# Kernel optimization log

Hardware: AMD Instinct MI355X
Metric: run time of the kernel (lower is better)

The kernel has to match this reference:

```python
import jax, jax.numpy as jnp
import numpy as np

B, S, D, H, FF = 2, 2048, 1024, 16, 4096
HD = D // H          # head dim = 64
ROT = HD // 2        # rotary dim = dim/(num_heads*2) = 32 (partial rotation)
EPS = 1e-5


def setup_inputs() -> dict:
    key = jax.random.key(0)
    ks = jax.random.split(key, 16)
    std = 0.02
    return {
        "x": jax.random.normal(ks[0], (B, S, D), jnp.float32),
        "mask": jnp.ones((B, 1, 1, S), jnp.int32),
        "wq": jax.random.normal(ks[1], (D, D), jnp.float32) * std,
        "bq": jnp.zeros((D,), jnp.float32),
        "wk": jax.random.normal(ks[2], (D, D), jnp.float32) * std,
        "bk": jnp.zeros((D,), jnp.float32),
        "wv": jax.random.normal(ks[3], (D, D), jnp.float32) * std,
        "bv": jnp.zeros((D,), jnp.float32),
        "wo": jax.random.normal(ks[4], (D, D), jnp.float32) * std,
        "bo": jnp.zeros((D,), jnp.float32),
        "ln1_w": jnp.ones((D,), jnp.float32),
        "ln1_b": jnp.zeros((D,), jnp.float32),
        "ln2_w": jnp.ones((D,), jnp.float32),
        "ln2_b": jnp.zeros((D,), jnp.float32),
        "w1": jax.random.normal(ks[5], (D, FF), jnp.float32) * std,
        "b1": jnp.zeros((FF,), jnp.float32),
        "w2": jax.random.normal(ks[6], (FF, D), jnp.float32) * std,
        "b2": jnp.zeros((D,), jnp.float32),
    }


def _layernorm(x, w, b):
    mu = jnp.mean(x, axis=-1, keepdims=True)
    var = jnp.mean(jnp.square(x - mu), axis=-1, keepdims=True)
    return (x - mu) * jax.lax.rsqrt(var + EPS) * w + b


def _rope(t):
    # t: [B, H, S, HD]; rotate first ROT features, interleaved (GPT-J) pairing
    inv_freq = 1.0 / (10000.0 ** (jnp.arange(0, ROT, 2, dtype=jnp.float32) / ROT))
    ang = jnp.arange(S, dtype=jnp.float32)[:, None] * inv_freq      # [S, ROT//2]
    ang = jnp.repeat(ang, 2, axis=-1)                               # [S, ROT]
    cos, sin = jnp.cos(ang), jnp.sin(ang)
    t_rot, t_pass = t[..., :ROT], t[..., ROT:]
    pr = t_rot.reshape(*t_rot.shape[:-1], ROT // 2, 2)
    rot = jnp.stack([-pr[..., 1], pr[..., 0]], axis=-1).reshape(t_rot.shape)
    return jnp.concatenate([t_rot * cos + rot * sin, t_pass], axis=-1)


def reference(x, mask, wq, bq, wk, bk, wv, bv, wo, bo,
              ln1_w, ln1_b, ln2_w, ln2_b, w1, b1, w2, b2):
    res = x
    h = _layernorm(x, ln1_w, ln1_b)
    q = (h @ wq + bq).reshape(B, S, H, HD).transpose(0, 2, 1, 3)
    k = (h @ wk + bk).reshape(B, S, H, HD).transpose(0, 2, 1, 3)
    v = (h @ wv + bv).reshape(B, S, H, HD).transpose(0, 2, 1, 3)
    q, k = _rope(q), _rope(k)
    score = jnp.einsum('bhqd,bhkd->bhqk', q, k) * (1.0 / np.sqrt(HD))
    score = jnp.where(mask == 0, jnp.float32(-1e9), score)
    attn = jax.nn.softmax(score, axis=-1)
    out = jnp.einsum('bhqk,bhkd->bhqd', attn, v)
    out = out.transpose(0, 2, 1, 3).reshape(B, S, D) @ wo + bo
    x = res + out
    res = x
    h = _layernorm(x, ln2_w, ln2_b)
    h = jax.nn.gelu(h @ w1 + b1, approximate=False) @ w2 + b2
    return res + h
```

## Files before the change

### kernel.cpp

```cpp
#include <hip/hip_runtime.h>
#include <cstdint>
#include <cstddef>


typedef __bf16 bf16;
typedef __bf16 bf16x2 __attribute__((ext_vector_type(2)));
typedef __bf16 bf16x4v __attribute__((ext_vector_type(4)));
typedef __bf16 bf16x8 __attribute__((ext_vector_type(8)));
typedef float  f32x4  __attribute__((ext_vector_type(4)));

#define NB 2
#define NS 2048
#define ND 1024
#define NH 16
#define NHD 64
#define NFF 4096
#define NM (NB*NS)
#define QKSCALE 0.18033688011112042f

typedef uint32_t __attribute__((address_space(1))) gu32_t;
typedef uint32_t __attribute__((address_space(3))) lu32_t;
__device__ __forceinline__ void async_copy16(void* lds, const void* g) {
  __builtin_amdgcn_global_load_lds((gu32_t*)g, (lu32_t*)lds, 16, 0, 0);
}

__device__ __forceinline__ float gelu_f(float x) {
  return 0.5f * x * (1.0f + erff(x * 0.70710678118654752f));
}

__global__ __launch_bounds__(256) void prep_kernel(
    const float* __restrict__ wq, const float* __restrict__ wk,
    const float* __restrict__ wv, const float* __restrict__ wo,
    const float* __restrict__ w1, const float* __restrict__ w2,
    bf16* __restrict__ wqt, bf16* __restrict__ wkt, bf16* __restrict__ wvt,
    bf16* __restrict__ wot, bf16* __restrict__ w1t, bf16* __restrict__ w2t,
    const float* __restrict__ bq, const float* __restrict__ bk,
    const float* __restrict__ bv, float* __restrict__ bcat,
    const int* __restrict__ mask, float* __restrict__ m01f,
    bf16* __restrict__ m01b, float2* __restrict__ rtab,
    const float* __restrict__ x, const float* __restrict__ ln1w,
    const float* __restrict__ ln1b, bf16* __restrict__ h1) {
  int flat = blockIdx.x;
  int t = threadIdx.x;
  if (flat < 12288) {
    __shared__ float tile[32][33];
    const float* W; bf16* Wt; long bx, by; int K, N;
    if (flat < 4096) {
      int which = flat >> 10, r = flat & 1023;
      const float* Ws[4] = {wq, wk, wv, wo};
      bf16* Wts[4] = {wqt, wkt, wvt, wot};
      W = Ws[which]; Wt = Wts[which]; bx = r & 31; by = r >> 5; K = ND; N = ND;
    } else if (flat < 8192) {
      int r = flat - 4096;
      W = w1; Wt = w1t; bx = r & 127; by = r >> 7; K = ND; N = NFF;
    } else {
      int r = flat - 8192;
      W = w2; Wt = w2t; bx = r & 31; by = r >> 5; K = NFF; N = ND;
    }
    int tx = t & 31, ty = t >> 5;
#pragma unroll
    for (int r = 0; r < 4; ++r)
      tile[ty + r*8][tx] = W[(by*32 + ty + r*8) * (long)N + bx*32 + tx];
    __syncthreads();
#pragma unroll
    for (int r = 0; r < 4; ++r)
      Wt[(bx*32 + ty + r*8) * (long)K + by*32 + tx] = (bf16)tile[tx][ty + r*8];
  } else if (flat < 12444) {
    int blk = flat - 12288;
    if (blk < 12) {
      int i = blk * 256 + t;
      bcat[i] = (i < ND) ? bq[i] : ((i < 2*ND) ? bk[i - ND] : bv[i - 2*ND]);
    } else if (blk < 28) {
      int i = (blk - 12) * 256 + t;
      float v = mask[i] ? 1.0f : 0.0f;
      m01f[i] = v;
      m01b[i] = (bf16)v;
    } else {
      int idx = (blk - 28) * 256 + t;
      int s = idx >> 4, i = idx & 15;
      float ang = (float)s * exp2f(-(float)i * (13.287712379549449f / 16.0f));
      float sn, cs;
      sincosf(ang, &sn, &cs);
      rtab[idx] = make_float2(cs, sn);
    }
  } else {
    long row = flat - 12444;
    float4 v = ((const float4*)(x + row*ND))[t];
    float s  = v.x + v.y + v.z + v.w;
    float sq = v.x*v.x + v.y*v.y + v.z*v.z + v.w*v.w;
#pragma unroll
    for (int m = 1; m <= 32; m <<= 1) { s += __shfl_xor(s, m); sq += __shfl_xor(sq, m); }
    __shared__ float ss[4], ssq[4];
    if ((t & 63) == 0) { ss[t>>6] = s; ssq[t>>6] = sq; }
    __syncthreads();
    s  = ss[0] + ss[1] + ss[2] + ss[3];
    sq = ssq[0] + ssq[1] + ssq[2] + ssq[3];
    float mu = s * (1.0f/ND);
    float rs = rsqrtf(sq * (1.0f/ND) - mu*mu + 1e-5f);
    float4 wv4 = ((const float4*)ln1w)[t];
    float4 bv4 = ((const float4*)ln1b)[t];
    bf16x4v o;
    o[0] = (bf16)((v.x-mu)*rs*wv4.x + bv4.x);
    o[1] = (bf16)((v.y-mu)*rs*wv4.y + bv4.y);
    o[2] = (bf16)((v.z-mu)*rs*wv4.z + bv4.z);
    o[3] = (bf16)((v.w-mu)*rs*wv4.w + bv4.w);
    *(bf16x4v*)(h1 + row*ND + t*4) = o;
  }
}

__global__ __launch_bounds__(256) void ln_kernel(
    const float* __restrict__ x, const float* __restrict__ w,
    const float* __restrict__ b, bf16* __restrict__ out) {
  long row = blockIdx.x;
  int t = threadIdx.x;
  float4 v = ((const float4*)(x + row*ND))[t];
  float s  = v.x + v.y + v.z + v.w;
  float sq = v.x*v.x + v.y*v.y + v.z*v.z + v.w*v.w;
#pragma unroll
  for (int m = 1; m <= 32; m <<= 1) { s += __shfl_xor(s, m); sq += __shfl_xor(sq, m); }
  __shared__ float ss[4], ssq[4];
  if ((t & 63) == 0) { ss[t>>6] = s; ssq[t>>6] = sq; }
  __syncthreads();
  s  = ss[0] + ss[1] + ss[2] + ss[3];
  sq = ssq[0] + ssq[1] + ssq[2] + ssq[3];
  float mu = s * (1.0f/ND);
  float rs = rsqrtf(sq * (1.0f/ND) - mu*mu + 1e-5f);
  float4 wv = ((const float4*)w)[t];
  float4 bv = ((const float4*)b)[t];
  bf16x4v o;
  o[0] = (bf16)((v.x-mu)*rs*wv.x + bv.x);
  o[1] = (bf16)((v.y-mu)*rs*wv.y + bv.y);
  o[2] = (bf16)((v.z-mu)*rs*wv.z + bv.z);
  o[3] = (bf16)((v.w-mu)*rs*wv.w + bv.w);
  *(bf16x4v*)(out + row*ND + t*4) = o;
}

template<int EPI>
__global__ __launch_bounds__(512, 2) void gemm256_kernel(
    const bf16* __restrict__ A, const bf16* __restrict__ Bt,
    const float* __restrict__ bias, void* __restrict__ Cout,
    const float2* __restrict__ rtab, const float* __restrict__ m01f,
    int M, int N, int K) {
  __shared__ __align__(16) bf16 Alds[4][256*32];
  __shared__ __align__(16) bf16 Blds[4][256*32];
  const int tid = threadIdx.x, lane = tid & 63, w = tid >> 6;
  const int fr = lane & 15, kg = lane >> 4;
  const int wr = w >> 2, wc = w & 3;
  const int swb = (kg ^ ((fr >> 1) & 3)) << 4;

  const int gx = gridDim.x;
  int lin = blockIdx.y * gx + blockIdx.x;
  int nwg = gx * gridDim.y;
  int swz = (lin & 7) * (nwg >> 3) + (lin >> 3);
  const long am0 = (long)(swz / gx) * 256;
  const long bn0 = (long)(swz % gx) * 256;

  const f32x4 fzero = {0.f, 0.f, 0.f, 0.f};
  f32x4 acc[8][4];
#pragma unroll
  for (int m = 0; m < 8; ++m)
#pragma unroll
    for (int n = 0; n < 4; ++n) acc[m][n] = fzero;

  auto stage = [&](int kt, int bufi) {
#pragma unroll
    for (int i = 0; i < 2; ++i) {
      int s = i*512 + tid;
      int r = s >> 2, c = (s & 3) ^ ((s >> 3) & 3);
      async_copy16((char*)&Alds[bufi][0] + i*8192 + w*1024,
                   &A[(am0 + r)*K + kt + c*8]);
      async_copy16((char*)&Blds[bufi][0] + i*8192 + w*1024,
                   &Bt[(bn0 + r)*K + kt + c*8]);
    }
  };

  const int nk = K >> 5;
  stage(0, 0);
  stage(32, 1);
  asm volatile("s_waitcnt vmcnt(4)" ::: "memory");
  __builtin_amdgcn_s_barrier();
  __builtin_amdgcn_sched_barrier(0);

  for (int t = 0; t < nk; ++t) {
    const int cur = t & 3;
    if (t + 2 < nk) stage((t + 2) * 32, (t + 2) & 3);
    const char* Ab = (const char*)&Alds[cur][0];
    const char* Bb = (const char*)&Blds[cur][0];
    bf16x8 af[4], bfv[4];
#pragma unroll
    for (int n = 0; n < 4; ++n) bfv[n] = *(const bf16x8*)(Bb + (wc*64 + n*16 + fr)*64 + swb);
#pragma unroll
    for (int m = 0; m < 4; ++m) af[m]  = *(const bf16x8*)(Ab + (wr*128 + m*16 + fr)*64 + swb);
    asm volatile("s_waitcnt lgkmcnt(0)" ::: "memory");
    __builtin_amdgcn_sched_barrier(0);
    __builtin_amdgcn_s_setprio(1);
#pragma unroll
    for (int m = 0; m < 4; ++m)
#pragma unroll
      for (int n = 0; n < 4; ++n)
        acc[m][n] = __builtin_amdgcn_mfma_f32_16x16x32_bf16(af[m], bfv[n], acc[m][n], 0, 0, 0);
    __builtin_amdgcn_s_setprio(0);
    __builtin_amdgcn_s_barrier();
#pragma unroll
    for (int m = 0; m < 4; ++m) af[m] = *(const bf16x8*)(Ab + (wr*128 + (m+4)*16 + fr)*64 + swb);
    asm volatile("s_waitcnt lgkmcnt(0)" ::: "memory");
    __builtin_amdgcn_sched_barrier(0);
    __builtin_amdgcn_s_setprio(1);
#pragma unroll
    for (int m = 0; m < 4; ++m)
#pragma unroll
      for (int n = 0; n < 4; ++n)
        acc[m+4][n] = __builtin_amdgcn_mfma_f32_16x16x32_bf16(af[m], bfv[n], acc[m+4][n], 0, 0, 0);
    __builtin_amdgcn_s_setprio(0);
    if (t + 2 < nk) { asm volatile("s_waitcnt vmcnt(4)" ::: "memory"); }
    else            { asm volatile("s_waitcnt vmcnt(0)" ::: "memory"); }
    __builtin_amdgcn_s_barrier();
    __builtin_amdgcn_sched_barrier(0);
  }

  const int rbase = kg * 4;
  const int region = (int)(bn0 >> 10);
#pragma unroll
  for (int m = 0; m < 8; ++m) {
#pragma unroll
    for (int n = 0; n < 4; ++n) {
      long col = bn0 + wc*64 + n*16 + fr;
      float bia = bias[col];
#pragma unroll
      for (int j = 0; j < 4; ++j) {
        long row = am0 + wr*128 + m*16 + rbase + j;
        float val = acc[m][n][j] + bia;
        if (EPI == 1) {
          ((bf16*)Cout)[row * N + col] = (bf16)gelu_f(val);
        } else {
          long cv = col & 1023;
          if (region <= 1) {
            float pval = __shfl_xor(val, 1);
            if (n < 2) {
              float2 cs = rtab[((row & (NS-1)) << 4) | ((n*16 + fr) >> 1)];
              val = (fr & 1) ? val*cs.x + pval*cs.y : val*cs.x - pval*cs.y;
            }
            if (region == 0) val *= QKSCALE;
            ((bf16*)Cout)[(long)region * (NM*(long)ND) + row * ND + cv] = (bf16)val;
          } else {
            val *= m01f[row];
            long vidx = (((row >> 11) << 4) | (cv >> 6)) * (64L*NS) + (cv & 63) * (long)NS + (row & 2047);
            ((bf16*)Cout)[2L * NM * ND + vidx] = (bf16)val;
          }
        }
      }
    }
  }
}

__global__ __launch_bounds__(512, 1) void gemm128x8_kernel(
    const bf16* __restrict__ A, const bf16* __restrict__ Bt,
    const float* __restrict__ bias, const float* __restrict__ res,
    float* __restrict__ Cout, int M, int N, int K) {
  __shared__ __align__(16) bf16 Alds[4][128*64];
  __shared__ __align__(16) bf16 Blds[4][128*64];
  const int tid = threadIdx.x, lane = tid & 63, w = tid >> 6;
  const int fr = lane & 15, kg = lane >> 4;
  const int wr = w >> 1, wc = w & 1;

  const int gx = gridDim.x;
  int lin = blockIdx.y * gx + blockIdx.x;
  int nwg = gx * gridDim.y;
  int swz = (lin & 7) * (nwg >> 3) + (lin >> 3);
  const long am0 = (long)(swz / gx) * 128;
  const long bn0 = (long)(swz % gx) * 128;

  const f32x4 fzero = {0.f, 0.f, 0.f, 0.f};
  f32x4 acc[2][4];
#pragma unroll
  for (int m = 0; m < 2; ++m)
#pragma unroll
    for (int n = 0; n < 4; ++n) acc[m][n] = fzero;

  auto stage = [&](int kt, int bufi) {
#pragma unroll
    for (int i = 0; i < 2; ++i) {
      int s = i*512 + tid;
      int r = s >> 3, c = (s & 7) ^ (r & 7);
      async_copy16((char*)&Alds[bufi][0] + i*8192 + w*1024,
                   &A[(am0 + r)*K + kt + c*8]);
      async_copy16((char*)&Blds[bufi][0] + i*8192 + w*1024,
                   &Bt[(bn0 + r)*K + kt + c*8]);
    }
  };

  const int nk = K >> 6;
  stage(0, 0);
  stage(64, 1);
  asm volatile("s_waitcnt vmcnt(4)" ::: "memory");
  __builtin_amdgcn_s_barrier();
  __builtin_amdgcn_sched_barrier(0);

  for (int t = 0; t < nk; ++t) {
    const int cur = t & 3;
    if (t + 2 < nk) stage((t + 2) * 64, (t + 2) & 3);
    const char* Ab = (const char*)&Alds[cur][0];
    const char* Bb = (const char*)&Blds[cur][0];
    bf16x8 af[2][2], bfv[2][4];
#pragma unroll
    for (int kk = 0; kk < 2; ++kk) {
#pragma unroll
      for (int m = 0; m < 2; ++m) {
        int r = wr*32 + m*16 + fr;
        af[kk][m] = *(const bf16x8*)(Ab + r*128 + (((kk*4 + kg) ^ (r & 7)) << 4));
      }
#pragma unroll
      for (int n = 0; n < 4; ++n) {
        int r = wc*64 + n*16 + fr;
        bfv[kk][n] = *(const bf16x8*)(Bb + r*128 + (((kk*4 + kg) ^ (r & 7)) << 4));
      }
    }
    asm volatile("s_waitcnt lgkmcnt(0)" ::: "memory");
    __builtin_amdgcn_sched_barrier(0);
    __builtin_amdgcn_s_setprio(1);
#pragma unroll
    for (int kk = 0; kk < 2; ++kk)
#pragma unroll
      for (int m = 0; m < 2; ++m)
#pragma unroll
        for (int n = 0; n < 4; ++n)
          acc[m][n] = __builtin_amdgcn_mfma_f32_16x16x32_bf16(af[kk][m], bfv[kk][n], acc[m][n], 0, 0, 0);
    __builtin_amdgcn_s_setprio(0);
    if (t + 2 < nk) { asm volatile("s_waitcnt vmcnt(4)" ::: "memory"); }
    else            { asm volatile("s_waitcnt vmcnt(0)" ::: "memory"); }
    __builtin_amdgcn_s_barrier();
    __builtin_amdgcn_sched_barrier(0);
  }

  const int rbase = kg * 4;
#pragma unroll
  for (int m = 0; m < 2; ++m) {
#pragma unroll
    for (int n = 0; n < 4; ++n) {
      long col = bn0 + wc*64 + n*16 + fr;
      float bia = bias[col];
#pragma unroll
      for (int j = 0; j < 4; ++j) {
        long row = am0 + wr*32 + m*16 + rbase + j;
        Cout[row * N + col] = acc[m][n][j] + bia + res[row * N + col];
      }
    }
  }
}

__global__ __launch_bounds__(512) void attn_kernel(
    const bf16* __restrict__ q, const bf16* __restrict__ k,
    const bf16* __restrict__ vt, const bf16* __restrict__ m01b,
    bf16* __restrict__ out) {
  int lin = blockIdx.y * 16 + blockIdx.x;
  int swz = (lin & 7) * 64 + (lin >> 3);
  const int qt = swz & 15;
  const int bh = swz >> 4;
  const int b = bh >> 4, h = bh & 15;
  const int tid = threadIdx.x, lane = tid & 63, w = tid >> 6;
  const int fr = lane & 15, kg = lane >> 4;
  const int k8 = kg * 8;
  const int frl = fr & 3, frh = fr >> 2;

  __shared__ __align__(16) bf16 Klds[3][64*64];
  __shared__ __align__(16) bf16 Vlds[3][64*64];
  __shared__ __align__(16) bf16 Mlds[NS];

  const long qrow = (long)qt*128 + w*16 + fr;
  const bf16* qbase = q + ((long)b*NS + qrow)*ND + h*NHD;
  bf16x8 qf[2];
  qf[0] = *(const bf16x8*)(qbase + k8);
  qf[1] = *(const bf16x8*)(qbase + 32 + k8);

  const bf16* kbase = k + (long)b*NS*ND + h*NHD;
  const bf16* vtb = vt + (long)bh*64*NS;
  const bf16* mbase = m01b + (long)b*NS;

  if (w < 4) async_copy16((char*)Mlds + w*1024, mbase + tid*8);

  const int srow = tid >> 3, sc = tid & 7;
  const int csK = (sc ^ (srow & 7) ^ (((srow >> 3) & 1) << 2));
  const int csV = (sc ^ (srow & 7));
  auto stageK = [&](int kt, int bufi) {
    async_copy16((char*)&Klds[bufi][0] + w*1024,
                 kbase + ((long)kt*64 + srow)*ND + csK*8);
  };
  auto stageV = [&](int kt, int bufi) {
    async_copy16((char*)&Vlds[bufi][0] + w*1024,
                 vtb + (long)srow*NS + kt*64 + csV*8);
  };

  const f32x4 fzero = {0.f, 0.f, 0.f, 0.f};
  f32x4 oacc[4], oaccL = fzero;
#pragma unroll
  for (int n = 0; n < 4; ++n) oacc[n] = fzero;

  stageK(0, 0); stageV(0, 0);
  stageK(1, 1); stageV(1, 1);
  asm volatile("s_waitcnt vmcnt(2)" ::: "memory");
  __builtin_amdgcn_s_barrier();
  __builtin_amdgcn_sched_barrier(0);

  const int NT = NS / 64;
  int bcur = 0, bpre = 1;
  for (int kt = 0; kt < NT; ++kt) {
    if (kt + 2 < NT) {
      bpre = (bpre == 2) ? 0 : bpre + 1;
      stageK(kt + 2, bpre);
      stageV(kt + 2, bpre);
    }
    const char* Kb = (const char*)&Klds[bcur][0];
    const char* Vb = (const char*)&Vlds[bcur][0];

    bf16x8 vbm0 = *(const bf16x8*)&Mlds[kt*64 + k8];
    bf16x8 vbm1 = *(const bf16x8*)&Mlds[kt*64 + 32 + k8];

    f32x4 sacc[4];
#pragma unroll
    for (int n = 0; n < 4; ++n) sacc[n] = fzero;
#pragma unroll
    for (int n = 0; n < 4; ++n) {
      int r = (frh << 3) + ((n & 1) << 2) + frl + ((n >> 1) << 5);
      int swzr = (r & 7) ^ (((r >> 3) & 1) << 2);
#pragma unroll
      for (int kk = 0; kk < 2; ++kk) {
        bf16x8 kf = *(const bf16x8*)(Kb + r*128 + ((((kk << 2) | kg) ^ swzr) << 4));
        sacc[n] = __builtin_amdgcn_mfma_f32_16x16x32_bf16(kf, qf[kk], sacc[n], 0, 0, 0);
      }
    }

    float p[4][4];
#pragma unroll
    for (int n = 0; n < 4; ++n) {
      p[n][0] = exp2f(sacc[n][0]);
      p[n][1] = exp2f(sacc[n][1]);
      p[n][2] = exp2f(sacc[n][2]);
      p[n][3] = exp2f(sacc[n][3]);
    }

    bf16x8 paf[2];
#pragma unroll
    for (int n = 0; n < 4; ++n) {
#pragma unroll
      for (int j = 0; j < 4; ++j)
        paf[n >> 1][((n & 1) << 2) + j] = (bf16)p[n][j];
    }

    oaccL = __builtin_amdgcn_mfma_f32_16x16x32_bf16(paf[0], vbm0, oaccL, 0, 0, 0);
    oaccL = __builtin_amdgcn_mfma_f32_16x16x32_bf16(paf[1], vbm1, oaccL, 0, 0, 0);

#pragma unroll
    for (int kk = 0; kk < 2; ++kk) {
#pragma unroll
      for (int n2 = 0; n2 < 4; ++n2) {
        int r = n2*16 + fr;
        bf16x8 vb8 = *(const bf16x8*)(Vb + r*128 + ((((kk << 2) | kg) ^ (r & 7)) << 4));
        oacc[n2] = __builtin_amdgcn_mfma_f32_16x16x32_bf16(paf[kk], vb8, oacc[n2], 0, 0, 0);
      }
    }

    if (kt + 2 < NT)      { asm volatile("s_waitcnt vmcnt(2)" ::: "memory"); }
    else if (kt + 1 < NT) { asm volatile("s_waitcnt vmcnt(0)" ::: "memory"); }
    __builtin_amdgcn_s_barrier();
    __builtin_amdgcn_sched_barrier(0);
    bcur = (bcur == 2) ? 0 : bcur + 1;
  }

#pragma unroll
  for (int j = 0; j < 4; ++j) {
    float inv = 1.0f / oaccL[j];
    long orow = (long)qt*128 + w*16 + kg*4 + j;
    bf16* ob = out + ((long)b*NS + orow)*ND + h*NHD;
#pragma unroll
    for (int n2 = 0; n2 < 4; ++n2) ob[n2*16 + fr] = (bf16)(oacc[n2][j] * inv);
  }
}

extern "C" void kernel_launch(void* const* d_in, const int* in_sizes, int n_in,
                              void* d_out, int out_size, void* d_ws, size_t ws_size,
                              hipStream_t stream) {
  const float* x    = (const float*)d_in[0];
  const int*   mask = (const int*)d_in[1];
  const float* wq   = (const float*)d_in[2];
  const float* bq   = (const float*)d_in[3];
  const float* wk   = (const float*)d_in[4];
  const float* bk   = (const float*)d_in[5];
  const float* wv   = (const float*)d_in[6];
  const float* bv   = (const float*)d_in[7];
  const float* wo   = (const float*)d_in[8];
  const float* bo   = (const float*)d_in[9];
  const float* ln1w = (const float*)d_in[10];
  const float* ln1b = (const float*)d_in[11];
  const float* ln2w = (const float*)d_in[12];
  const float* ln2b = (const float*)d_in[13];
  const float* w1   = (const float*)d_in[14];
  const float* b1   = (const float*)d_in[15];
  const float* w2   = (const float*)d_in[16];
  const float* b2   = (const float*)d_in[17];
  float* out = (float*)d_out;

  char* ws = (char*)d_ws;
  const size_t MB = 1024ull * 1024ull;
  bf16* wqt = (bf16*)(ws + 0*MB);
  bf16* wkt = (bf16*)(ws + 2*MB);
  bf16* wvt = (bf16*)(ws + 4*MB);
  bf16* wot = (bf16*)(ws + 6*MB);
  bf16* w1t = (bf16*)(ws + 8*MB);
  bf16* w2t = (bf16*)(ws + 16*MB);
  bf16* h1   = (bf16*)(ws + 24*MB);
  bf16* qb   = (bf16*)(ws + 32*MB);
  bf16* kb   = (bf16*)(ws + 40*MB);
  bf16* vtb  = (bf16*)(ws + 48*MB);
  bf16* attn = h1;
  bf16* f1   = (bf16*)(ws + 24*MB);
  float* y1  = (float*)(ws + 56*MB);
  bf16* h2   = (bf16*)(ws + 72*MB);
  float* bcat = (float*)(ws + 80*MB);
  float* m01f = (float*)(ws + 80*MB + 16*1024);
  bf16*  m01b = (bf16*) (ws + 80*MB + 32*1024);
  float2* rtab = (float2*)(ws + 80*MB + 48*1024);
  (void)in_sizes; (void)n_in; (void)out_size; (void)ws_size;

  prep_kernel<<<16540, 256, 0, stream>>>(wq, wk, wv, wo, w1, w2,
                                         wqt, wkt, wvt, wot, w1t, w2t,
                                         bq, bk, bv, bcat, mask, m01f, m01b,
                                         rtab, x, ln1w, ln1b, h1);

  gemm256_kernel<3><<<dim3(12, 16), 512, 0, stream>>>(h1, wqt, bcat, qb,
                                                      rtab, m01f, NM, 3*ND, ND);
  attn_kernel<<<dim3(16, 32), 512, 0, stream>>>(qb, kb, vtb, m01b, attn);

  gemm128x8_kernel<<<dim3(8, 32), 512, 0, stream>>>(attn, wot, bo, x, y1,
                                                    NM, ND, ND);
  ln_kernel<<<NM, 256, 0, stream>>>(y1, ln2w, ln2b, h2);
  gemm256_kernel<1><<<dim3(16, 16), 512, 0, stream>>>(h2, w1t, b1, f1,
                                                      nullptr, nullptr, NM, NFF, ND);
  gemm128x8_kernel<<<dim3(8, 32), 512, 0, stream>>>(f1, w2t, b2, y1, out,
                                                    NM, ND, NFF);
}
```

Before: 308.3 us.

## Write V row-major from QKV GEMM, add separate transpose kernel, double-buffer LDS

The QKV GEMM epilogue now writes V in the same row-major layout as Q and K, replacing the scattered transposed store. A new tiled transpose kernel then produces the V^T layout the attention kernel expects. The 256-tile GEMM also drops from a 4-buffer, 2-ahead LDS pipeline to a 2-buffer, 1-ahead one with a full vmcnt(0) wait each iteration, which halves LDS use but reduces prefetch depth. Workspace aliasing changes so that V^T lives in the h1 buffer and the attention output goes to a new region.

```diff
diff --git a/kernel.cpp b/kernel.cpp
--- a/kernel.cpp
+++ b/kernel.cpp
@@ -108,6 +108,27 @@
   }
 }
 
+__global__ __launch_bounds__(256) void vtrans_kernel(
+    const bf16* __restrict__ v, bf16* __restrict__ vt) {
+  __shared__ bf16 t[64][66];
+  int st = blockIdx.x, bh = blockIdx.y;
+  int b = bh >> 4, h = bh & 15;
+  int c = threadIdx.x & 63, rg = threadIdx.x >> 6;
+  const bf16* src = v + ((long)b*NS + st*64)*ND + h*64;
+#pragma unroll
+  for (int i = 0; i < 16; ++i) {
+    int r = rg*16 + i;
+    t[r][c] = src[(long)r*ND + c];
+  }
+  __syncthreads();
+  bf16* dst = vt + (long)bh*64*NS + st*64;
+#pragma unroll
+  for (int i = 0; i < 16; ++i) {
+    int d = rg*16 + i;
+    dst[(long)d*NS + c] = t[c][d];
+  }
+}
+
 __global__ __launch_bounds__(256) void ln_kernel(
     const float* __restrict__ x, const float* __restrict__ w,
     const float* __restrict__ b, bf16* __restrict__ out) {
@@ -141,8 +162,8 @@
     const float* __restrict__ bias, void* __restrict__ Cout,
     const float2* __restrict__ rtab, const float* __restrict__ m01f,
     int M, int N, int K) {
-  __shared__ __align__(16) bf16 Alds[4][256*32];
-  __shared__ __align__(16) bf16 Blds[4][256*32];
+  __shared__ __align__(16) bf16 Alds[2][256*32];
+  __shared__ __align__(16) bf16 Blds[2][256*32];
   const int tid = threadIdx.x, lane = tid & 63, w = tid >> 6;
   const int fr = lane & 15, kg = lane >> 4;
   const int wr = w >> 2, wc = w & 3;
@@ -176,14 +197,13 @@
 
   const int nk = K >> 5;
   stage(0, 0);
-  stage(32, 1);
-  asm volatile("s_waitcnt vmcnt(4)" ::: "memory");
+  asm volatile("s_waitcnt vmcnt(0)" ::: "memory");
   __builtin_amdgcn_s_barrier();
   __builtin_amdgcn_sched_barrier(0);
 
   for (int t = 0; t < nk; ++t) {
-    const int cur = t & 3;
-    if (t + 2 < nk) stage((t + 2) * 32, (t + 2) & 3);
+    const int cur = t & 1;
+    if (t + 1 < nk) stage((t + 1) * 32, cur ^ 1);
     const char* Ab = (const char*)&Alds[cur][0];
     const char* Bb = (const char*)&Blds[cur][0];
     bf16x8 af[4], bfv[4];
@@ -200,7 +220,6 @@
       for (int n = 0; n < 4; ++n)
         acc[m][n] = __builtin_amdgcn_mfma_f32_16x16x32_bf16(af[m], bfv[n], acc[m][n], 0, 0, 0);
     __builtin_amdgcn_s_setprio(0);
-    __builtin_amdgcn_s_barrier();
 #pragma unroll
     for (int m = 0; m < 4; ++m) af[m] = *(const bf16x8*)(Ab + (wr*128 + (m+4)*16 + fr)*64 + swb);
     asm volatile("s_waitcnt lgkmcnt(0)" ::: "memory");
@@ -212,8 +231,7 @@
       for (int n = 0; n < 4; ++n)
         acc[m+4][n] = __builtin_amdgcn_mfma_f32_16x16x32_bf16(af[m], bfv[n], acc[m+4][n], 0, 0, 0);
     __builtin_amdgcn_s_setprio(0);
-    if (t + 2 < nk) { asm volatile("s_waitcnt vmcnt(4)" ::: "memory"); }
-    else            { asm volatile("s_waitcnt vmcnt(0)" ::: "memory"); }
+    asm volatile("s_waitcnt vmcnt(0)" ::: "memory");
     __builtin_amdgcn_s_barrier();
     __builtin_amdgcn_sched_barrier(0);
   }
@@ -241,12 +259,10 @@
               val = (fr & 1) ? val*cs.x + pval*cs.y : val*cs.x - pval*cs.y;
             }
             if (region == 0) val *= QKSCALE;
-            ((bf16*)Cout)[(long)region * (NM*(long)ND) + row * ND + cv] = (bf16)val;
           } else {
             val *= m01f[row];
-            long vidx = (((row >> 11) << 4) | (cv >> 6)) * (64L*NS) + (cv & 63) * (long)NS + (row & 2047);
-            ((bf16*)Cout)[2L * NM * ND + vidx] = (bf16)val;
           }
+          ((bf16*)Cout)[(long)region * (NM*(long)ND) + row * ND + cv] = (bf16)val;
         }
       }
     }
@@ -510,8 +526,9 @@
   bf16* h1   = (bf16*)(ws + 24*MB);
   bf16* qb   = (bf16*)(ws + 32*MB);
   bf16* kb   = (bf16*)(ws + 40*MB);
-  bf16* vtb  = (bf16*)(ws + 48*MB);
-  bf16* attn = h1;
+  bf16* vb   = (bf16*)(ws + 48*MB);
+  bf16* vtb  = h1;
+  bf16* attnb = (bf16*)(ws + 72*MB);
   bf16* f1   = (bf16*)(ws + 24*MB);
   float* y1  = (float*)(ws + 56*MB);
   bf16* h2   = (bf16*)(ws + 72*MB);
@@ -528,9 +545,11 @@
 
   gemm256_kernel<3><<<dim3(12, 16), 512, 0, stream>>>(h1, wqt, bcat, qb,
                                                       rtab, m01f, NM, 3*ND, ND);
-  attn_kernel<<<dim3(16, 32), 512, 0, stream>>>(qb, kb, vtb, m01b, attn);
-
-  gemm128x8_kernel<<<dim3(8, 32), 512, 0, stream>>>(attn, wot, bo, x, y1,
+  vtrans_kernel<<<dim3(32, 32), 256, 0, stream>>>(vb, vtb);
+
+  attn_kernel<<<dim3(16, 32), 512, 0, stream>>>(qb, kb, vtb, m01b, attnb);
+
+  gemm128x8_kernel<<<dim3(8, 32), 512, 0, stream>>>(attnb, wot, bo, x, y1,
                                                     NM, ND, ND);
   ln_kernel<<<NM, 256, 0, stream>>>(y1, ln2w, ln2b, h2);
   gemm256_kernel<1><<<dim3(16, 16), 512, 0, stream>>>(h2, w1t, b1, f1,
```

Result: faster. 289.5 us (-6.1%).
